# Optimization experiments

Hardware: AMD Instinct MI355X
Metric: run time of the kernel (lower is better)

The kernel has to match this reference:

```python
import jax, jax.numpy as jnp
import numpy as np

N_NODES = 50000
N_EDGES = 800000
DIM_IN, DIM_H, DIM_OUT = 96, 128, 16


def setup_inputs() -> dict:
    key = jax.random.key(0)
    ks = jax.random.split(key, 8)
    x = jax.random.normal(ks[0], (N_NODES, DIM_IN), dtype=jnp.float32)
    edge_index = jax.random.randint(ks[1], (2, N_EDGES), 0, N_NODES, dtype=jnp.int64)
    W1_l = jax.random.normal(ks[2], (DIM_IN, DIM_H), dtype=jnp.float32) * 0.1
    b1_l = jax.random.normal(ks[3], (DIM_H,), dtype=jnp.float32) * 0.1
    W1_r = jax.random.normal(ks[4], (DIM_IN, DIM_H), dtype=jnp.float32) * 0.1
    W2_l = jax.random.normal(ks[5], (DIM_H, DIM_OUT), dtype=jnp.float32) * 0.1
    b2_l = jax.random.normal(ks[6], (DIM_OUT,), dtype=jnp.float32) * 0.1
    W2_r = jax.random.normal(ks[7], (DIM_H, DIM_OUT), dtype=jnp.float32) * 0.1
    return {"x": x, "edge_index": edge_index, "W1_l": W1_l, "b1_l": b1_l,
            "W1_r": W1_r, "W2_l": W2_l, "b2_l": b2_l, "W2_r": W2_r}


def _mean_aggregate(x, src, dst, n_nodes):
    # gather neighbor features along edges, mean-reduce at destination nodes
    msgs = x[src]                                      # [E, d]
    agg = jax.ops.segment_sum(msgs, dst, num_segments=n_nodes)  # [N, d]
    deg = jax.ops.segment_sum(jnp.ones_like(src, dtype=x.dtype), dst,
                              num_segments=n_nodes)    # [N]
    return agg / jnp.maximum(deg, 1.0)[:, None]


def _sage_conv(x, src, dst, W_l, b_l, W_r):
    # PyG SAGEConv (mean aggr): lin_l(mean_j x_j) + lin_r(x); bias on lin_l only
    agg = _mean_aggregate(x, src, dst, x.shape[0])
    return agg @ W_l + b_l + x @ W_r


def reference(x, edge_index, W1_l, b1_l, W1_r, W2_l, b2_l, W2_r):
    src, dst = edge_index[0], edge_index[1]
    h = jax.nn.relu(_sage_conv(x, src, dst, W1_l, b1_l, W1_r))
    h = _sage_conv(h, src, dst, W2_l, b2_l, W2_r)
    return jax.nn.softmax(h, axis=1)
```

## Files before the change

kernel.cpp:

```cpp
#include <hip/hip_runtime.h>

#define NN 50000
#define NE 800000
#define DIN 96
#define DH 128
#define DOUT 16
#define NBKT ((NN + 127) / 128)
#define CAPB 2560
#define EPB 2048
#define NSLC ((NE + EPB - 1) / EPB)
#define SLICE 24
#define QSCALE (5.0f / 127.0f)
#define QINV (127.0f / 5.0f)

typedef __attribute__((ext_vector_type(8))) short bf16x8;
typedef __attribute__((ext_vector_type(4))) float f32x4;
typedef unsigned short ushort_t;

__device__ inline short f2bf(float f) {
    unsigned u = __float_as_uint(f);
    u += 0x7fff + ((u >> 16) & 1);
    return (short)(u >> 16);
}
__device__ inline float bflo(unsigned u) { return __uint_as_float(u << 16); }
__device__ inline float bfhi(unsigned u) { return __uint_as_float(u & 0xffff0000u); }
__device__ inline unsigned char q8(float f) {
    float v = fminf(fmaxf(f * QINV, -127.f), 127.f);
    return (unsigned char)(signed char)(int)rintf(v);
}

#define XB_BLOCKS ((NN * DIN / 4 + 511) / 512)
#define WC_BLOCKS ((DH * 192 + 32 * DH + 511) / 512)
__global__ __launch_bounds__(512) void k_prep(const float* __restrict__ x,
                                              const float* __restrict__ W1l,
                                              const float* __restrict__ W1r,
                                              const float* __restrict__ W2l,
                                              const float* __restrict__ W2r,
                                              const int* __restrict__ ei,
                                              short* __restrict__ xb,
                                              unsigned char* __restrict__ xq,
                                              short* __restrict__ Bt,
                                              short* __restrict__ Bt2,
                                              unsigned* __restrict__ bpack,
                                              int* __restrict__ scnt) {
    __shared__ unsigned stage[EPB];
    __shared__ int bcnt[NBKT];
    __shared__ int bfil[NBKT];
    __shared__ int brun[NBKT];
    __shared__ int sbuf[512];
    const int tid = threadIdx.x;

    if (blockIdx.x < XB_BLOCKS) {
        int i = blockIdx.x * 512 + tid;
        if (i < NN * DIN / 4) {
            float4 v = ((const float4*)x)[i];
            short4 o;
            o.x = f2bf(v.x); o.y = f2bf(v.y); o.z = f2bf(v.z); o.w = f2bf(v.w);
            ((short4*)xb)[i] = o;
            uchar4 qo;
            qo.x = q8(v.x); qo.y = q8(v.y); qo.z = q8(v.z); qo.w = q8(v.w);
            ((uchar4*)xq)[i] = qo;
        }
        return;
    }
    if (blockIdx.x < XB_BLOCKS + WC_BLOCKS) {
        int idx = (blockIdx.x - XB_BLOCKS) * 512 + tid;
        if (idx < DH * 192) {
            int n = idx / 192, kk = idx % 192;
            float v = (kk < DIN) ? W1l[kk * DH + n] : W1r[(kk - DIN) * DH + n];
            Bt[idx] = f2bf(v);
        } else if (idx < DH * 192 + 32 * DH) {
            int j = idx - DH * 192;
            int c = j >> 7, k = j & 127;
            float v = (c < DOUT) ? W2l[k * DOUT + c] : W2r[k * DOUT + (c - DOUT)];
            Bt2[j] = f2bf(v);
        }
        return;
    }
    const int j = blockIdx.x - XB_BLOCKS - WC_BLOCKS;
    const int e0 = j * EPB;
    const int ecnt = min(EPB, NE - e0);
    for (int i = tid; i < NBKT; i += 512) { bcnt[i] = 0; bfil[i] = 0; }
    __syncthreads();
    unsigned dcache[EPB / 512];
#pragma unroll
    for (int k = 0; k < EPB / 512; ++k) {
        int i = tid + k * 512;
        if (i < ecnt) {
            unsigned d = (unsigned)ei[NE + e0 + i];
            dcache[k] = d;
            atomicAdd(&bcnt[d >> 7], 1);
        }
    }
    __syncthreads();
    int v = (tid < NBKT) ? bcnt[tid] : 0;
    sbuf[tid] = v;
    __syncthreads();
    for (int o = 1; o < 512; o <<= 1) {
        int tv = (tid >= o) ? sbuf[tid - o] : 0;
        __syncthreads();
        sbuf[tid] += tv;
        __syncthreads();
    }
    if (tid < NBKT) brun[tid] = sbuf[tid] - v;
    __syncthreads();
#pragma unroll
    for (int k = 0; k < EPB / 512; ++k) {
        int i = tid + k * 512;
        if (i < ecnt) {
            unsigned s = (unsigned)ei[e0 + i];
            unsigned d = dcache[k];
            int b = d >> 7;
            int p = atomicAdd(&bfil[b], 1);
            stage[brun[b] + p] = (d << 16) | s;
        }
    }
    __syncthreads();
    for (int i = tid; i < ecnt; i += 512) {
        unsigned p = stage[i];
        int b = p >> 23;
        int idx = i - brun[b];
        if (idx < SLICE)
            bpack[((size_t)j * NBKT + b) * SLICE + idx] = p;
    }
    for (int b = tid; b < NBKT; b += 512)
        scnt[j * NBKT + b] = min(bcnt[b], SLICE);
}

__global__ __launch_bounds__(512) void k_build(const unsigned* __restrict__ bpack,
                                               const int* __restrict__ scnt,
                                               int* __restrict__ offs,
                                               int* __restrict__ offe,
                                               ushort_t* __restrict__ csr) {
    __shared__ unsigned pairs[CAPB];
    __shared__ int scl[NSLC];
    __shared__ int sbs[NSLC];
    __shared__ int sbuf[512];
    __shared__ int ncnt[128];
    __shared__ int nrun[128];
    __shared__ int lcur[128];
    __shared__ int cnt_s;
    const int bkt = blockIdx.x;
    const int tid = threadIdx.x;

    for (int j = tid; j < NSLC; j += 512) scl[j] = scnt[j * NBKT + bkt];
    if (tid < 128) { ncnt[tid] = 0; lcur[tid] = 0; }
    __syncthreads();
    int v = (tid < NSLC) ? scl[tid] : 0;
    sbuf[tid] = v;
    __syncthreads();
    for (int o = 1; o < 512; o <<= 1) {
        int tv = (tid >= o) ? sbuf[tid - o] : 0;
        __syncthreads();
        sbuf[tid] += tv;
        __syncthreads();
    }
    if (tid < NSLC) sbs[tid] = sbuf[tid] - v;
    if (tid == NSLC - 1) cnt_s = sbuf[tid];
    __syncthreads();
    const int cnt = min(cnt_s, CAPB);

    for (int idx = tid; idx < NSLC * SLICE; idx += 512) {
        int j = idx / SLICE, k = idx - j * SLICE;
        if (k < scl[j]) {
            int pos = sbs[j] + k;
            if (pos < CAPB)
                pairs[pos] = bpack[((size_t)j * NBKT + bkt) * SLICE + k];
        }
    }
    __syncthreads();

    for (int i = tid; i < cnt; i += 512)
        atomicAdd(&ncnt[(pairs[i] >> 16) & 127], 1);
    __syncthreads();
    v = (tid < 128) ? ncnt[tid] : 0;
    sbuf[tid] = v;
    __syncthreads();
    for (int o = 1; o < 128; o <<= 1) {
        int tv = (tid >= o && tid < 128) ? sbuf[tid - o] : 0;
        __syncthreads();
        if (tid < 128) sbuf[tid] += tv;
        __syncthreads();
    }
    if (tid < 128) {
        nrun[tid] = sbuf[tid] - v;
        const int n = bkt * 128 + tid;
        if (n < NN) {
            offs[n] = bkt * CAPB + nrun[tid];
            offe[n] = bkt * CAPB + nrun[tid] + v;
        }
    }
    __syncthreads();
    for (int i = tid; i < cnt; i += 512) {
        unsigned p = pairs[i];
        int nd = (p >> 16) & 127;
        int pos = atomicAdd(&lcur[nd], 1);
        csr[(size_t)bkt * CAPB + nrun[nd] + pos] = (ushort_t)(p & 0xffffu);
    }
}

__global__ __launch_bounds__(256) void k_agg1(const unsigned char* __restrict__ xq,
                                              const ushort_t* __restrict__ csr,
                                              const int* __restrict__ offs,
                                              const int* __restrict__ offe,
                                              short* __restrict__ m1b) {
    const int w = threadIdx.x >> 6;
    const int l = threadIdx.x & 63;
    const int n = blockIdx.x * 4 + w;
    if (n >= NN) return;
    const int eg = l / 12;
    const int c  = l % 12;
    const int b = offs[n], e = offe[n];
    const uint2* xr = (const uint2*)xq;
    int acc[8];
#pragma unroll
    for (int k = 0; k < 8; ++k) acc[k] = 0;
    int i = (eg < 4) ? b + eg : e;
    for (; i + 12 < e; i += 16) {
        uint2 u0 = xr[(size_t)csr[i]      * 12 + c];
        uint2 u1 = xr[(size_t)csr[i + 4]  * 12 + c];
        uint2 u2 = xr[(size_t)csr[i + 8]  * 12 + c];
        uint2 u3 = xr[(size_t)csr[i + 12] * 12 + c];
#pragma unroll
        for (int k = 0; k < 4; ++k) {
            acc[k]     += (int)(signed char)(u0.x >> (8 * k)) + (int)(signed char)(u1.x >> (8 * k))
                        + (int)(signed char)(u2.x >> (8 * k)) + (int)(signed char)(u3.x >> (8 * k));
            acc[4 + k] += (int)(signed char)(u0.y >> (8 * k)) + (int)(signed char)(u1.y >> (8 * k))
                        + (int)(signed char)(u2.y >> (8 * k)) + (int)(signed char)(u3.y >> (8 * k));
        }
    }
    for (; i < e; i += 4) {
        uint2 u0 = xr[(size_t)csr[i] * 12 + c];
#pragma unroll
        for (int k = 0; k < 4; ++k) {
            acc[k]     += (int)(signed char)(u0.x >> (8 * k));
            acc[4 + k] += (int)(signed char)(u0.y >> (8 * k));
        }
    }
#pragma unroll
    for (int k = 0; k < 8; ++k) acc[k] += __shfl(acc[k], l + 24);
#pragma unroll
    for (int k = 0; k < 8; ++k) acc[k] += __shfl(acc[k], l + 12);
    if (l < 12) {
        const float sc = (e > b) ? QSCALE / (float)(e - b) : 0.0f;
        unsigned op[4];
#pragma unroll
        for (int jj = 0; jj < 4; ++jj)
            op[jj] = (unsigned)(unsigned short)f2bf((float)acc[2 * jj] * sc)
                   | ((unsigned)(unsigned short)f2bf((float)acc[2 * jj + 1] * sc) << 16);
        ((uint4*)m1b)[(size_t)n * 12 + l] = make_uint4(op[0], op[1], op[2], op[3]);
    }
}

#define SHP 136
__global__ __launch_bounds__(256) void k_linproj(const short* __restrict__ m1b,
                                                 const short* __restrict__ xb,
                                                 const short* __restrict__ Bt,
                                                 const float* __restrict__ b1,
                                                 const short* __restrict__ Bt2,
                                                 const float* __restrict__ b2,
                                                 short* __restrict__ zlb,
                                                 float* __restrict__ s) {
    __shared__ __align__(16) short sh[64][SHP];
    const int w = threadIdx.x >> 6;
    const int l = threadIdx.x & 63;
    const int lr = l & 15;
    const int lk = l >> 4;
    int row = blockIdx.x * 64 + w * 16 + lr;
    if (row >= NN) row = NN - 1;

    f32x4 acc[8];
#pragma unroll
    for (int nt = 0; nt < 8; ++nt) {
        float bv = b1[nt * 16 + lr];
        acc[nt] = (f32x4){bv, bv, bv, bv};
    }
    bf16x8 afr[6];
    {
        const bf16x8* am = (const bf16x8*)(m1b + (size_t)row * DIN);
        const bf16x8* ax = (const bf16x8*)(xb  + (size_t)row * DIN);
        afr[0] = am[lk];     afr[1] = am[4 + lk]; afr[2] = am[8 + lk];
        afr[3] = ax[lk];     afr[4] = ax[4 + lk]; afr[5] = ax[8 + lk];
    }
    const bf16x8* bt8 = (const bf16x8*)Bt;
#pragma unroll
    for (int st = 0; st < 6; ++st) {
#pragma unroll
        for (int nt = 0; nt < 8; ++nt) {
            bf16x8 bfr = bt8[(size_t)(nt * 16 + lr) * 24 + st * 4 + lk];
            acc[nt] = __builtin_amdgcn_mfma_f32_16x16x32_bf16(afr[st], bfr, acc[nt], 0, 0, 0);
        }
    }
    const int lrow0 = w * 16 + lk * 4;
#pragma unroll
    for (int r = 0; r < 4; ++r) {
#pragma unroll
        for (int nt = 0; nt < 8; ++nt)
            sh[lrow0 + r][nt * 16 + lr] = f2bf(fmaxf(acc[nt][r], 0.f));
    }
    __syncthreads();

    bf16x8 pafr[4];
#pragma unroll
    for (int st = 0; st < 4; ++st)
        pafr[st] = *(const bf16x8*)&sh[w * 16 + lr][st * 32 + lk * 8];

    f32x4 accz = (f32x4){0.f, 0.f, 0.f, 0.f};
    float bv = b2[lr];
    f32x4 accs = (f32x4){bv, bv, bv, bv};
    const bf16x8* b8 = (const bf16x8*)Bt2;
#pragma unroll
    for (int st = 0; st < 4; ++st) {
        bf16x8 bz = b8[(size_t)lr * 16 + st * 4 + lk];
        bf16x8 bs = b8[(size_t)(16 + lr) * 16 + st * 4 + lk];
        accz = __builtin_amdgcn_mfma_f32_16x16x32_bf16(pafr[st], bz, accz, 0, 0, 0);
        accs = __builtin_amdgcn_mfma_f32_16x16x32_bf16(pafr[st], bs, accs, 0, 0, 0);
    }
    const int orow0 = blockIdx.x * 64 + w * 16 + lk * 4;
#pragma unroll
    for (int r = 0; r < 4; ++r) {
        const int orow = orow0 + r;
        if (orow < NN) {
            zlb[(size_t)orow * DOUT + lr] = f2bf(accz[r]);
            s[(size_t)orow * DOUT + lr] = accs[r];
        }
    }
}

__global__ __launch_bounds__(256) void k_agg2(const short* __restrict__ zlb,
                                              const float* __restrict__ s,
                                              const ushort_t* __restrict__ csr,
                                              const int* __restrict__ offs,
                                              const int* __restrict__ offe,
                                              float* __restrict__ out) {
    const int w = threadIdx.x >> 6;
    const int lane = threadIdx.x & 63;
    const int n = blockIdx.x * 4 + w;
    if (n >= NN) return;
    const int b = offs[n], e = offe[n];
    const int ng = lane >> 2;
    const int sl = lane & 3;
    const uint2* z2 = (const uint2*)zlb;
    float4 acc = {0.f, 0.f, 0.f, 0.f};
    for (int i = b + ng; i < e; i += 16) {
        uint2 u = z2[(size_t)csr[i] * 4 + sl];
        acc.x += bflo(u.x);
        acc.y += bfhi(u.x);
        acc.z += bflo(u.y);
        acc.w += bfhi(u.y);
    }
#pragma unroll
    for (int o = 4; o <= 32; o <<= 1) {
        acc.x += __shfl_xor(acc.x, o);
        acc.y += __shfl_xor(acc.y, o);
        acc.z += __shfl_xor(acc.z, o);
        acc.w += __shfl_xor(acc.w, o);
    }
    const float inv = (e > b) ? 1.0f / (float)(e - b) : 0.0f;
    const float4 sv = ((const float4*)s)[(size_t)n * 4 + sl];
    float4 v;
    v.x = acc.x * inv + sv.x;
    v.y = acc.y * inv + sv.y;
    v.z = acc.z * inv + sv.z;
    v.w = acc.w * inv + sv.w;
    float mx = fmaxf(fmaxf(v.x, v.y), fmaxf(v.z, v.w));
    mx = fmaxf(mx, __shfl_xor(mx, 1));
    mx = fmaxf(mx, __shfl_xor(mx, 2));
    v.x = expf(v.x - mx); v.y = expf(v.y - mx);
    v.z = expf(v.z - mx); v.w = expf(v.w - mx);
    float sm = v.x + v.y + v.z + v.w;
    sm += __shfl_xor(sm, 1);
    sm += __shfl_xor(sm, 2);
    const float r = 1.0f / sm;
    v.x *= r; v.y *= r; v.z *= r; v.w *= r;
    if (ng == 0) ((float4*)out)[(size_t)n * 4 + sl] = v;
}

template <typename T>
static inline T* align_up(void* p, size_t a = 64) {
    return (T*)(((uintptr_t)p + (a - 1)) & ~(uintptr_t)(a - 1));
}

extern "C" void kernel_launch(void* const* d_in, const int* in_sizes, int n_in,
                              void* d_out, int out_size, void* d_ws, size_t ws_size,
                              hipStream_t stream) {
    const float* x   = (const float*)d_in[0];
    const int*   ei  = (const int*)d_in[1];
    const float* W1l = (const float*)d_in[2];
    const float* b1  = (const float*)d_in[3];
    const float* W1r = (const float*)d_in[4];
    const float* W2l = (const float*)d_in[5];
    const float* b2  = (const float*)d_in[6];
    const float* W2r = (const float*)d_in[7];
    float* out = (float*)d_out;

    unsigned* bpack = (unsigned*)d_ws;
    int* scnt     = (int*)(bpack + (size_t)NSLC * NBKT * SLICE);
    float* s      = (float*)(scnt + (size_t)NSLC * NBKT);
    int* offs     = (int*)(s + (size_t)NN * DOUT);
    int* offe     = offs + NN;
    ushort_t* csr = (ushort_t*)align_up<short>(offe + NN);
    short* xb     = (short*)csr + (size_t)NBKT * CAPB;
    short* m1b    = xb + (size_t)NN * DIN;
    short* zlb    = m1b + (size_t)NN * DIN;
    short* Bt     = zlb + (size_t)NN * DOUT;
    short* Bt2    = Bt + (size_t)DH * 192;
    unsigned char* xq = align_up<unsigned char>(Bt2 + 32 * DH);

    k_prep<<<XB_BLOCKS + WC_BLOCKS + NSLC, 512, 0, stream>>>(
        x, W1l, W1r, W2l, W2r, ei, xb, xq, Bt, Bt2, bpack, scnt);
    k_build<<<NBKT, 512, 0, stream>>>(bpack, scnt, offs, offe, csr);
    k_agg1<<<(NN + 3) / 4, 256, 0, stream>>>(xq, csr, offs, offe, m1b);
    k_linproj<<<(NN + 63) / 64, 256, 0, stream>>>(m1b, xb, Bt, b1, Bt2, b2, zlb, s);
    k_agg2<<<(NN + 3) / 4, 256, 0, stream>>>(zlb, s, csr, offs, offe, out);
}
```

Baseline: 109.7 us.

## Split int8 feature table into two column halves and aggregate each in separate passes

The quantized node features are stored as two separate 48-byte-per-row tables, one per column half, and layer-1 aggregation runs as two kernel launches, each gathering one half. The intent is that each pass's gather working set (2.4 MB instead of 4.8 MB) fits better in L2/MALL, which should raise hit rates for the random neighbor gathers. The cost is reading the CSR and offsets twice, an extra launch, and narrower 4-byte loads per lane in place of 8-byte loads.

```diff
diff --git a/kernel.cpp b/kernel.cpp
--- a/kernel.cpp
+++ b/kernel.cpp
@@ -38,7 +38,8 @@
                                               const float* __restrict__ W2r,
                                               const int* __restrict__ ei,
                                               short* __restrict__ xb,
-                                              unsigned char* __restrict__ xq,
+                                              unsigned char* __restrict__ xqA,
+                                              unsigned char* __restrict__ xqB,
                                               short* __restrict__ Bt,
                                               short* __restrict__ Bt2,
                                               unsigned* __restrict__ bpack,
@@ -59,7 +60,9 @@
             ((short4*)xb)[i] = o;
             uchar4 qo;
             qo.x = q8(v.x); qo.y = q8(v.y); qo.z = q8(v.z); qo.w = q8(v.w);
-            ((uchar4*)xq)[i] = qo;
+            const int row = i / 24, q = i % 24;
+            if (q < 12) ((uchar4*)xqA)[row * 12 + q] = qo;
+            else        ((uchar4*)xqB)[row * 12 + (q - 12)] = qo;
         }
         return;
     }
@@ -199,11 +202,12 @@
     }
 }
 
-__global__ __launch_bounds__(256) void k_agg1(const unsigned char* __restrict__ xq,
-                                              const ushort_t* __restrict__ csr,
-                                              const int* __restrict__ offs,
-                                              const int* __restrict__ offe,
-                                              short* __restrict__ m1b) {
+template <int H>
+__global__ __launch_bounds__(256) void k_agg1h(const unsigned char* __restrict__ xh,
+                                               const ushort_t* __restrict__ csr,
+                                               const int* __restrict__ offs,
+                                               const int* __restrict__ offe,
+                                               short* __restrict__ m1b) {
     const int w = threadIdx.x >> 6;
     const int l = threadIdx.x & 63;
     const int n = blockIdx.x * 4 + w;
@@ -211,44 +215,38 @@
     const int eg = l / 12;
     const int c  = l % 12;
     const int b = offs[n], e = offe[n];
-    const uint2* xr = (const uint2*)xq;
-    int acc[8];
-#pragma unroll
-    for (int k = 0; k < 8; ++k) acc[k] = 0;
+    const unsigned* xr = (const unsigned*)xh;
+    int acc[4];
+#pragma unroll
+    for (int k = 0; k < 4; ++k) acc[k] = 0;
     int i = (eg < 4) ? b + eg : e;
     for (; i + 12 < e; i += 16) {
-        uint2 u0 = xr[(size_t)csr[i]      * 12 + c];
-        uint2 u1 = xr[(size_t)csr[i + 4]  * 12 + c];
-        uint2 u2 = xr[(size_t)csr[i + 8]  * 12 + c];
-        uint2 u3 = xr[(size_t)csr[i + 12] * 12 + c];
-#pragma unroll
-        for (int k = 0; k < 4; ++k) {
-            acc[k]     += (int)(signed char)(u0.x >> (8 * k)) + (int)(signed char)(u1.x >> (8 * k))
-                        + (int)(signed char)(u2.x >> (8 * k)) + (int)(signed char)(u3.x >> (8 * k));
-            acc[4 + k] += (int)(signed char)(u0.y >> (8 * k)) + (int)(signed char)(u1.y >> (8 * k))
-                        + (int)(signed char)(u2.y >> (8 * k)) + (int)(signed char)(u3.y >> (8 * k));
-        }
+        unsigned u0 = xr[(size_t)csr[i]      * 12 + c];
+        unsigned u1 = xr[(size_t)csr[i + 4]  * 12 + c];
+        unsigned u2 = xr[(size_t)csr[i + 8]  * 12 + c];
+        unsigned u3 = xr[(size_t)csr[i + 12] * 12 + c];
+#pragma unroll
+        for (int k = 0; k < 4; ++k)
+            acc[k] += (int)(signed char)(u0 >> (8 * k)) + (int)(signed char)(u1 >> (8 * k))
+                    + (int)(signed char)(u2 >> (8 * k)) + (int)(signed char)(u3 >> (8 * k));
     }
     for (; i < e; i += 4) {
-        uint2 u0 = xr[(size_t)csr[i] * 12 + c];
-#pragma unroll
-        for (int k = 0; k < 4; ++k) {
-            acc[k]     += (int)(signed char)(u0.x >> (8 * k));
-            acc[4 + k] += (int)(signed char)(u0.y >> (8 * k));
-        }
-    }
-#pragma unroll
-    for (int k = 0; k < 8; ++k) acc[k] += __shfl(acc[k], l + 24);
-#pragma unroll
-    for (int k = 0; k < 8; ++k) acc[k] += __shfl(acc[k], l + 12);
+        unsigned u0 = xr[(size_t)csr[i] * 12 + c];
+#pragma unroll
+        for (int k = 0; k < 4; ++k)
+            acc[k] += (int)(signed char)(u0 >> (8 * k));
+    }
+#pragma unroll
+    for (int k = 0; k < 4; ++k) acc[k] += __shfl(acc[k], l + 24);
+#pragma unroll
+    for (int k = 0; k < 4; ++k) acc[k] += __shfl(acc[k], l + 12);
     if (l < 12) {
         const float sc = (e > b) ? QSCALE / (float)(e - b) : 0.0f;
-        unsigned op[4];
-#pragma unroll
-        for (int jj = 0; jj < 4; ++jj)
-            op[jj] = (unsigned)(unsigned short)f2bf((float)acc[2 * jj] * sc)
-                   | ((unsigned)(unsigned short)f2bf((float)acc[2 * jj + 1] * sc) << 16);
-        ((uint4*)m1b)[(size_t)n * 12 + l] = make_uint4(op[0], op[1], op[2], op[3]);
+        unsigned o0 = (unsigned)(unsigned short)f2bf((float)acc[0] * sc)
+                    | ((unsigned)(unsigned short)f2bf((float)acc[1] * sc) << 16);
+        unsigned o1 = (unsigned)(unsigned short)f2bf((float)acc[2] * sc)
+                    | ((unsigned)(unsigned short)f2bf((float)acc[3] * sc) << 16);
+        *(uint2*)&m1b[(size_t)n * DIN + H * 48 + 4 * l] = make_uint2(o0, o1);
     }
 }
 
@@ -405,12 +403,14 @@
     short* zlb    = m1b + (size_t)NN * DIN;
     short* Bt     = zlb + (size_t)NN * DOUT;
     short* Bt2    = Bt + (size_t)DH * 192;
-    unsigned char* xq = align_up<unsigned char>(Bt2 + 32 * DH);
+    unsigned char* xqA = align_up<unsigned char>(Bt2 + 32 * DH);
+    unsigned char* xqB = xqA + (size_t)NN * 48;
 
     k_prep<<<XB_BLOCKS + WC_BLOCKS + NSLC, 512, 0, stream>>>(
-        x, W1l, W1r, W2l, W2r, ei, xb, xq, Bt, Bt2, bpack, scnt);
+        x, W1l, W1r, W2l, W2r, ei, xb, xqA, xqB, Bt, Bt2, bpack, scnt);
     k_build<<<NBKT, 512, 0, stream>>>(bpack, scnt, offs, offe, csr);
-    k_agg1<<<(NN + 3) / 4, 256, 0, stream>>>(xq, csr, offs, offe, m1b);
+    k_agg1h<0><<<(NN + 3) / 4, 256, 0, stream>>>(xqA, csr, offs, offe, m1b);
+    k_agg1h<1><<<(NN + 3) / 4, 256, 0, stream>>>(xqB, csr, offs, offe, m1b);
     k_linproj<<<(NN + 63) / 64, 256, 0, stream>>>(m1b, xb, Bt, b1, Bt2, b2, zlb, s);
     k_agg2<<<(NN + 3) / 4, 256, 0, stream>>>(zlb, s, csr, offs, offe, out);
 }
```

After: 121.6 us. 1.11x slower.
